# Kernel optimization log

Hardware: AMD Instinct MI355X
Metric: run time of the kernel (lower is better)

The kernel has to match this reference:

```python
import jax, jax.numpy as jnp
import numpy as np


def setup_inputs() -> dict:
    key = jax.random.key(0)
    ka, kb = jax.random.split(key)
    B, S, I, J = 8, 8192, 256, 256
    a = jax.random.normal(ka, (B, S, I), dtype=jnp.float32)
    b = jax.random.normal(kb, (B, S, J), dtype=jnp.float32)
    return {"a": a, "b": b}


def reference(a, b):
    # mean_s(a_si outer b_sj) == (a^T @ b) / s, without materializing [*, i, j, s]
    s = a.shape[-2]
    out = jnp.einsum('...si,...sj->...ij', a, b) / s  # [*, i, j]
    return out
```

## Files before the change

kernel.cpp:

```cpp
#include <hip/hip_runtime.h>
#include <hip/hip_bf16.h>

typedef __bf16 bf16x8 __attribute__((ext_vector_type(8)));
typedef float f32x16 __attribute__((ext_vector_type(16)));
typedef float f32x4 __attribute__((ext_vector_type(4)));

#define S_TOTAL 8192
#define DIM 256
#define BK 32

__global__ __launch_bounds__(1024) void opm_partial(
    const float* __restrict__ A, const float* __restrict__ Bm,
    __bf16* __restrict__ dstbf, float* __restrict__ dstf32,
    int split, int kc, float scale)
{
    __shared__ float ldsA[2][BK][DIM];
    __shared__ float ldsB[2][BK][DIM];

    const int tid = threadIdx.x;
    const int w   = tid >> 6;
    const int l   = tid & 63;
    const int batch = blockIdx.x / split;
    const int sp    = blockIdx.x % split;
    const long long base = (long long)batch * S_TOTAL * DIM;
    const int s0 = sp * kc;
    const int wr = w >> 2, wc = w & 3;
    const int lane31 = l & 31;
    const int hi = l >> 5;
    const int niter = kc / BK;

    f32x16 acc[2][2] = {};

    auto stage = [&](int buf, int it) {
        #pragma unroll
        for (int q = 0; q < 4; ++q) {
            const int g = w * 4 + q;
            const int r = g & 31;
            const long long s = (long long)s0 + (long long)it * BK + r;
            const float* gp;
            const float* lp;
            if (g < 32) { gp = A  + base + s * DIM + l * 4; lp = &ldsA[buf][r][0]; }
            else        { gp = Bm + base + s * DIM + l * 4; lp = &ldsB[buf][r][0]; }
            __builtin_amdgcn_global_load_lds(
                (const __attribute__((address_space(1))) unsigned int*)gp,
                (__attribute__((address_space(3))) unsigned int*)lp, 16, 0, 0);
        }
    };

    auto compute = [&](int buf) {
        #pragma unroll
        for (int t = 0; t < 2; ++t) {
            const int srow = t * 16 + hi * 8;
            bf16x8 af[2], bfv[2];
            #pragma unroll
            for (int mi = 0; mi < 2; ++mi) {
                const int i = wr * 64 + mi * 32 + lane31;
                #pragma unroll
                for (int e = 0; e < 8; ++e)
                    af[mi][e] = (__bf16)ldsA[buf][srow + e][i];
            }
            #pragma unroll
            for (int nj = 0; nj < 2; ++nj) {
                const int j = wc * 64 + nj * 32 + lane31;
                #pragma unroll
                for (int e = 0; e < 8; ++e)
                    bfv[nj][e] = (__bf16)ldsB[buf][srow + e][j];
            }
            #pragma unroll
            for (int mi = 0; mi < 2; ++mi)
                #pragma unroll
                for (int nj = 0; nj < 2; ++nj)
                    acc[mi][nj] = __builtin_amdgcn_mfma_f32_32x32x16_bf16(
                        af[mi], bfv[nj], acc[mi][nj], 0, 0, 0);
        }
    };

    stage(0, 0);
    for (int it = 0; it < niter; ++it) {
        const int cur = it & 1;
        if (it + 1 < niter) {
            stage(cur ^ 1, it + 1);
            asm volatile("s_waitcnt vmcnt(4)" ::: "memory");
        } else {
            asm volatile("s_waitcnt vmcnt(0)" ::: "memory");
        }
        __builtin_amdgcn_s_barrier();
        __builtin_amdgcn_sched_barrier(0);
        compute(cur);
        __builtin_amdgcn_sched_barrier(0);
        __builtin_amdgcn_s_barrier();
    }

    if (dstf32) {
        float* o = dstf32 + (long long)blockIdx.x * (256 * 256);
        #pragma unroll
        for (int mi = 0; mi < 2; ++mi)
        #pragma unroll
        for (int nj = 0; nj < 2; ++nj)
        #pragma unroll
        for (int r = 0; r < 16; ++r) {
            const int row = (r & 3) + 8 * (r >> 2) + 4 * hi;
            const int i = wr * 64 + mi * 32 + row;
            const int j = wc * 64 + nj * 32 + lane31;
            o[i * 256 + j] = acc[mi][nj][r] * scale;
        }
    } else {
        __bf16* o = dstbf + (long long)blockIdx.x * (256 * 256);
        #pragma unroll
        for (int mi = 0; mi < 2; ++mi)
        #pragma unroll
        for (int nj = 0; nj < 2; ++nj)
        #pragma unroll
        for (int r = 0; r < 16; ++r) {
            const int row = (r & 3) + 8 * (r >> 2) + 4 * hi;
            const int i = wr * 64 + mi * 32 + row;
            const int j = wc * 64 + nj * 32 + lane31;
            o[i * 256 + j] = (__bf16)(acc[mi][nj][r] * scale);
        }
    }
}

__global__ __launch_bounds__(256) void opm_reduce(
    const __bf16* __restrict__ ws, float* __restrict__ out, int split)
{
    const int idx = blockIdx.x * 256 + threadIdx.x;
    const int b = idx >> 13;
    const int r = idx & 8191;
    const bf16x8* p = (const bf16x8*)ws + (long long)b * split * 8192 + r;
    float s[8] = {0.f, 0.f, 0.f, 0.f, 0.f, 0.f, 0.f, 0.f};
    for (int sp = 0; sp < split; ++sp) {
        bf16x8 v = p[(long long)sp * 8192];
        #pragma unroll
        for (int e = 0; e < 8; ++e) s[e] += (float)v[e];
    }
    f32x4 lo = { s[0], s[1], s[2], s[3] };
    f32x4 hiv = { s[4], s[5], s[6], s[7] };
    lo  *= (1.0f / 8192.0f);
    hiv *= (1.0f / 8192.0f);
    ((f32x4*)out)[idx * 2]     = lo;
    ((f32x4*)out)[idx * 2 + 1] = hiv;
}

extern "C" void kernel_launch(void* const* d_in, const int* in_sizes, int n_in,
                              void* d_out, int out_size, void* d_ws, size_t ws_size,
                              hipStream_t stream)
{
    (void)in_sizes; (void)n_in; (void)out_size;
    const float* A  = (const float*)d_in[0];
    const float* Bm = (const float*)d_in[1];
    float* out = (float*)d_out;

    int split = 32;
    while (split > 1 && (size_t)8 * split * 65536 * sizeof(__bf16) > ws_size) split >>= 1;

    if (split >= 2) {
        const int kc = S_TOTAL / split;
        opm_partial<<<8 * split, 1024, 0, stream>>>(A, Bm, (__bf16*)d_ws, nullptr, split, kc, 1.0f);
        opm_reduce<<<256, 256, 0, stream>>>((const __bf16*)d_ws, out, split);
    } else {
        opm_partial<<<8, 1024, 0, stream>>>(A, Bm, nullptr, out, 1, S_TOTAL, 1.0f / 8192.0f);
    }
}
```

Measured before the change: 41.76 us.

## Convert inputs to bf16 once in registers and store MFMA-ready LDS layout

Replaces direct global-to-LDS fp32 staging with register loads that are converted to bf16 once and written to LDS in a k-packed layout. MFMA operands then come from single 16-byte LDS reads instead of eight scalar fp32 reads plus conversions per fragment. BK grows to 64 and the pipeline becomes register-prefetch with a single LDS buffer per matrix. This removes redundant per-wave conversions and scalar LDS reads, but uses scalar strided global loads (coalesced across lanes), adds an extra barrier per iteration, and increases register pressure.

```diff
diff --git a/kernel.cpp b/kernel.cpp
--- a/kernel.cpp
+++ b/kernel.cpp
@@ -1,5 +1,4 @@
 #include <hip/hip_runtime.h>
-#include <hip/hip_bf16.h>
 
 typedef __bf16 bf16x8 __attribute__((ext_vector_type(8)));
 typedef float f32x16 __attribute__((ext_vector_type(16)));
@@ -7,15 +6,14 @@
 
 #define S_TOTAL 8192
 #define DIM 256
-#define BK 32
+#define BK 64
 
 __global__ __launch_bounds__(1024) void opm_partial(
     const float* __restrict__ A, const float* __restrict__ Bm,
     __bf16* __restrict__ dstbf, float* __restrict__ dstf32,
     int split, int kc, float scale)
 {
-    __shared__ float ldsA[2][BK][DIM];
-    __shared__ float ldsB[2][BK][DIM];
+    __shared__ __bf16 lds[2][8 * 256 * 8];
 
     const int tid = threadIdx.x;
     const int w   = tid >> 6;
@@ -29,43 +27,42 @@
     const int hi = l >> 5;
     const int niter = kc / BK;
 
+    const int mat = w >> 3;
+    const int kb  = w & 7;
+    const float* src = mat ? Bm : A;
+    __bf16* dstl = &lds[mat][0];
+
     f32x16 acc[2][2] = {};
+    float r[32];
 
-    auto stage = [&](int buf, int it) {
+    auto loadreg = [&](int it) {
+        const long long rowbase = base + (long long)(s0 + it * BK + kb * 8) * DIM + l;
         #pragma unroll
-        for (int q = 0; q < 4; ++q) {
-            const int g = w * 4 + q;
-            const int r = g & 31;
-            const long long s = (long long)s0 + (long long)it * BK + r;
-            const float* gp;
-            const float* lp;
-            if (g < 32) { gp = A  + base + s * DIM + l * 4; lp = &ldsA[buf][r][0]; }
-            else        { gp = Bm + base + s * DIM + l * 4; lp = &ldsB[buf][r][0]; }
-            __builtin_amdgcn_global_load_lds(
-                (const __attribute__((address_space(1))) unsigned int*)gp,
-                (__attribute__((address_space(3))) unsigned int*)lp, 16, 0, 0);
+        for (int c = 0; c < 4; ++c)
+            #pragma unroll
+            for (int e = 0; e < 8; ++e)
+                r[c * 8 + e] = src[rowbase + e * DIM + c * 64];
+    };
+    auto cvtwrite = [&]() {
+        #pragma unroll
+        for (int c = 0; c < 4; ++c) {
+            bf16x8 v;
+            #pragma unroll
+            for (int e = 0; e < 8; ++e) v[e] = (__bf16)r[c * 8 + e];
+            *(bf16x8*)&dstl[(kb * 256 + l + c * 64) * 8] = v;
         }
     };
-
-    auto compute = [&](int buf) {
+    auto compute = [&]() {
         #pragma unroll
-        for (int t = 0; t < 2; ++t) {
-            const int srow = t * 16 + hi * 8;
+        for (int t = 0; t < 4; ++t) {
+            const int kb0 = t * 2 + hi;
             bf16x8 af[2], bfv[2];
             #pragma unroll
-            for (int mi = 0; mi < 2; ++mi) {
-                const int i = wr * 64 + mi * 32 + lane31;
-                #pragma unroll
-                for (int e = 0; e < 8; ++e)
-                    af[mi][e] = (__bf16)ldsA[buf][srow + e][i];
-            }
+            for (int mi = 0; mi < 2; ++mi)
+                af[mi] = *(const bf16x8*)&lds[0][(kb0 * 256 + wr * 64 + mi * 32 + lane31) * 8];
             #pragma unroll
-            for (int nj = 0; nj < 2; ++nj) {
-                const int j = wc * 64 + nj * 32 + lane31;
-                #pragma unroll
-                for (int e = 0; e < 8; ++e)
-                    bfv[nj][e] = (__bf16)ldsB[buf][srow + e][j];
-            }
+            for (int nj = 0; nj < 2; ++nj)
+                bfv[nj] = *(const bf16x8*)&lds[1][(kb0 * 256 + wc * 64 + nj * 32 + lane31) * 8];
             #pragma unroll
             for (int mi = 0; mi < 2; ++mi)
                 #pragma unroll
@@ -75,20 +72,19 @@
         }
     };
 
-    stage(0, 0);
+    loadreg(0);
+    cvtwrite();
+    __syncthreads();
+
     for (int it = 0; it < niter; ++it) {
-        const int cur = it & 1;
+        if (it + 1 < niter) loadreg(it + 1);
+        __builtin_amdgcn_sched_barrier(0);
+        compute();
+        __syncthreads();
         if (it + 1 < niter) {
-            stage(cur ^ 1, it + 1);
-            asm volatile("s_waitcnt vmcnt(4)" ::: "memory");
-        } else {
-            asm volatile("s_waitcnt vmcnt(0)" ::: "memory");
+            cvtwrite();
+            __syncthreads();
         }
-        __builtin_amdgcn_s_barrier();
-        __builtin_amdgcn_sched_barrier(0);
-        compute(cur);
-        __builtin_amdgcn_sched_barrier(0);
-        __builtin_amdgcn_s_barrier();
     }
 
     if (dstf32) {
@@ -98,11 +94,11 @@
         #pragma unroll
         for (int nj = 0; nj < 2; ++nj)
         #pragma unroll
-        for (int r = 0; r < 16; ++r) {
-            const int row = (r & 3) + 8 * (r >> 2) + 4 * hi;
+        for (int q = 0; q < 16; ++q) {
+            const int row = (q & 3) + 8 * (q >> 2) + 4 * hi;
             const int i = wr * 64 + mi * 32 + row;
             const int j = wc * 64 + nj * 32 + lane31;
-            o[i * 256 + j] = acc[mi][nj][r] * scale;
+            o[i * 256 + j] = acc[mi][nj][q] * scale;
         }
     } else {
         __bf16* o = dstbf + (long long)blockIdx.x * (256 * 256);
@@ -111,11 +107,11 @@
         #pragma unroll
         for (int nj = 0; nj < 2; ++nj)
         #pragma unroll
-        for (int r = 0; r < 16; ++r) {
-            const int row = (r & 3) + 8 * (r >> 2) + 4 * hi;
+        for (int q = 0; q < 16; ++q) {
+            const int row = (q & 3) + 8 * (q >> 2) + 4 * hi;
             const int i = wr * 64 + mi * 32 + row;
             const int j = wc * 64 + nj * 32 + lane31;
-            o[i * 256 + j] = (__bf16)(acc[mi][nj][r] * scale);
+            o[i * 256 + j] = (__bf16)(acc[mi][nj][q] * scale);
         }
     }
 }
```

Result: slower. 42.68 us (+2.2%).
